# Kernel optimization log

Measured on AMD Instinct MI355X. Metric: run time of the kernel, lower is better.

The kernel has to match this reference:

```python
import jax, jax.numpy as jnp
from jax import lax
import numpy as np

EPS = 0.1          # DBSCAN radius (init arg eps)
MIN_SAMPLES = 5    # DBSCAN min_samples (init arg min_samples)
NC_MAX = 512       # fixed padded cluster budget (8 per dim * 64 dims)


def _dbscan_1d(x):
    """Exact 1-D DBSCAN on a vector x of shape (N,).
    Returns (labels, n_clusters). labels[i] in [-1, n_clusters), -1 = noise.
    Clusters are numbered in ascending value order (canonical deterministic
    relabeling of sklearn's discovery order). Border points are attached to
    the nearest core point (ties -> left)."""
    n = x.shape[0]
    order = jnp.argsort(x)
    xs = x[order]
    # core test: #points within [xs-eps, xs+eps] >= min_samples
    hi = jnp.searchsorted(xs, xs + EPS, side='right')
    lo = jnp.searchsorted(xs, xs - EPS, side='left')
    core = (hi - lo) >= MIN_SAMPLES
    inf = jnp.inf
    core_vals = jnp.where(core, xs, -inf)
    run_max = lax.cummax(core_vals, axis=0)                 # nearest core value to the left (incl self)
    prev_core_val = jnp.concatenate([jnp.full((1,), -inf, xs.dtype), run_max[:-1]])
    # a core point starts a new cluster iff no core point within eps on its left
    new_cluster = core & ((xs - prev_core_val) > EPS)
    starts = jnp.cumsum(new_cluster.astype(jnp.int32))
    cid = starts - 1                                        # cluster id carried along sorted order
    ncl = starts[-1]
    # nearest core on the left / right (values and their cluster ids)
    left_cid = lax.cummax(jnp.where(core, cid, -1), axis=0)
    left_val = run_max
    right_cid = lax.cummin(jnp.where(core, cid, n + 1), axis=0, reverse=True)
    right_val = lax.cummin(jnp.where(core, xs, inf), axis=0, reverse=True)
    dl = xs - left_val
    dr = right_val - xs
    border_cid = jnp.where(dl <= dr, left_cid, right_cid)
    border_ok = jnp.minimum(dl, dr) <= EPS
    lab_sorted = jnp.where(core, cid, jnp.where(border_ok, border_cid, -1))
    labels = jnp.zeros_like(lab_sorted).at[order].set(lab_sorted)  # unsort to original node order
    return labels, ncl


def setup_inputs() -> dict:
    key = jax.random.key(0)
    features = jax.random.normal(key, (8, 16384, 64), dtype=jnp.float32)
    return {"features": features}


def reference(features):
    B, N, D = features.shape
    xt = jnp.transpose(features, (0, 2, 1))                  # (B, D, N)
    labels, ncl = jax.vmap(jax.vmap(_dbscan_1d))(xt)         # (B, D, N), (B, D)
    off = jnp.cumsum(ncl, axis=1) - ncl                      # exclusive prefix: global cluster offset per dim
    glb = jnp.where(labels >= 0, labels + off[:, :, None], -1)
    # noise / overflow -> dump into padding column NC_MAX, sliced off below
    lbl = jnp.where(glb >= 0, jnp.minimum(glb, NC_MAX), NC_MAX)
    inc = jnp.zeros((B, N, NC_MAX + 1), features.dtype)
    b_ix = jnp.arange(B)[:, None, None]
    n_ix = jnp.arange(N)[None, None, :]
    inc = inc.at[b_ix, n_ix, lbl].set(1.0)                   # scatter cluster membership
    return inc[:, :, :NC_MAX]                                # (B, N, NC_MAX) padded incidence matrix
```

## Files before the change

kernel.cpp:

```cpp
#include <hip/hip_runtime.h>

#define NPTS   16384
#define NDIM   64
#define NBATCH 8
#define TB     1024
#define VPT    16
#define NB     8192
#define BPT    8
#define EPSF   0.1f
#define MINS   5
#define NCMAX  512
#define BIGI   0x3fffffff

__device__ __forceinline__ int phys(int i)  { return i ^ ((i >> 5) & 15); }
__device__ __forceinline__ int lphys(int i) { return i ^ (((i >> 6) & 31) << 1); }

__device__ __forceinline__ int binof(float x, float mn, float inv) {
  float fb = (x - mn) * inv;
  int b = (int)fb;
  if (fb < 0.f) b = 0;
  if (b > NB - 1) b = NB - 1;
  return b;
}

__global__ void ktrans(const float* __restrict__ f, float* __restrict__ xt) {
  __shared__ float tile[64][65];
  int blk = blockIdx.x;
  int b   = blk >> 8;
  int n0  = (blk & 255) << 6;
  for (int i = threadIdx.x; i < 64 * 64; i += 256) {
    int n = i >> 6, d = i & 63;
    tile[n][d] = f[((size_t)b * NPTS + n0 + n) * NDIM + d];
  }
  __syncthreads();
  for (int i = threadIdx.x; i < 64 * 64; i += 256) {
    int d = i >> 6, n = i & 63;
    xt[((size_t)b * NDIM + d) * NPTS + n0 + n] = tile[n][d];
  }
}

struct FS { int h; float f; float l; int li; int c; };
__device__ __forceinline__ FS fsid() { FS r; r.h = 0; r.f = 0.f; r.l = 0.f; r.li = -1; r.c = 0; return r; }
__device__ __forceinline__ FS fscomb(FS a, FS b) {
  FS r;
  r.h  = a.h | b.h;
  r.f  = a.h ? a.f : b.f;
  r.l  = b.h ? b.l : a.l;
  r.li = b.h ? b.li : a.li;
  int gap = (a.h && b.h && ((b.f - a.l) > EPSF)) ? 1 : 0;
  r.c  = a.c + b.c + gap;
  return r;
}

__global__ void __launch_bounds__(TB) kdbscan(const float* __restrict__ xt,
                                              short* __restrict__ labels,
                                              int* __restrict__ nclg) {
  const int tid  = threadIdx.x;
  const int lane = tid & 63;
  const int wid  = tid >> 6;
  const int bd   = blockIdx.x;
  const float* __restrict__ x = xt + (size_t)bd * NPTS;

  __shared__ float xs[NPTS];
  __shared__ unsigned int hist[NB];
  __shared__ unsigned int offs[NB];
  __shared__ float wmn[16], wmx[16];
  __shared__ unsigned int wsum[16];
  __shared__ int   sh[16];  __shared__ float sf[16], sl[16];
  __shared__ int   sli[16]; __shared__ int   sc[16];
  __shared__ int   wri[16]; __shared__ float wrv[16];
  short* lab = (short*)hist;

  float v[VPT];
  float mn = INFINITY, mx = -INFINITY;
  #pragma unroll
  for (int s = 0; s < VPT; ++s) {
    v[s] = x[tid + s * TB];
    mn = fminf(mn, v[s]); mx = fmaxf(mx, v[s]);
  }
  for (int d = 1; d < 64; d <<= 1) {
    mn = fminf(mn, __shfl_xor(mn, d));
    mx = fmaxf(mx, __shfl_xor(mx, d));
  }
  if (lane == 0) { wmn[wid] = mn; wmx[wid] = mx; }
  __syncthreads();
  mn = wmn[0]; mx = wmx[0];
  for (int w = 1; w < 16; ++w) { mn = fminf(mn, wmn[w]); mx = fmaxf(mx, wmx[w]); }
  float range = mx - mn;
  float inv = (range > 0.f) ? ((float)NB / range) : 0.f;

  for (int i = tid; i < NB; i += TB) hist[i] = 0u;
  __syncthreads();
  #pragma unroll
  for (int s = 0; s < VPT; ++s) atomicAdd(&hist[binof(v[s], mn, inv)], 1u);
  __syncthreads();

  unsigned int loc[BPT];
  unsigned int run = 0;
  const int bbase = tid * BPT;
  #pragma unroll
  for (int j = 0; j < BPT; ++j) { loc[j] = run; run += hist[bbase + j]; }
  unsigned int incl = run;
  for (int d = 1; d < 64; d <<= 1) {
    unsigned int u = __shfl_up(incl, d);
    if (lane >= d) incl += u;
  }
  unsigned int exc = __shfl_up(incl, 1);
  if (lane == 0) exc = 0u;
  if (lane == 63) wsum[wid] = incl;
  __syncthreads();
  unsigned int wb = 0;
  for (int w = 0; w < wid; ++w) wb += wsum[w];
  unsigned int tb0 = wb + exc;
  #pragma unroll
  for (int j = 0; j < BPT; ++j) offs[bbase + j] = tb0 + loc[j];
  __syncthreads();

  int pos[VPT];
  #pragma unroll
  for (int s = 0; s < VPT; ++s) {
    int b = binof(v[s], mn, inv);
    int p = (int)atomicAdd(&offs[b], 1u);
    pos[s] = p;
    xs[phys(p)] = v[s];
  }
  __syncthreads();

  int tgt[VPT];
  #pragma unroll
  for (int s = 0; s < VPT; ++s) {
    int b  = binof(v[s], mn, inv);
    int e0 = (int)offs[b];
    int s0 = e0 - (int)hist[b];
    float vv = v[s]; int pp = pos[s];
    int r = 0;
    for (int j = s0; j < e0; ++j) {
      float xj = xs[phys(j)];
      r += (xj < vv || (xj == vv && j < pp)) ? 1 : 0;
    }
    tgt[s] = s0 + r;
  }
  __syncthreads();
  #pragma unroll
  for (int s = 0; s < VPT; ++s) xs[phys(tgt[s])] = v[s];
  __syncthreads();

  const int p0 = tid * VPT;
  float w[VPT + 8];
  #pragma unroll
  for (int k = 0; k < VPT + 8; ++k) {
    int i = p0 - 4 + k;
    w[k] = (i < 0) ? -INFINITY : ((i >= NPTS) ? INFINITY : xs[phys(i)]);
  }
  unsigned int coremask = 0u;
  #pragma unroll
  for (int s = 0; s < VPT; ++s) {
    float xi = w[s + 4];
    float lo = xi - EPSF, hi = xi + EPSF;
    bool core = false;
    #pragma unroll
    for (int t = 0; t < MINS; ++t)
      core |= (w[s + 4 - t] >= lo) && (w[s + 8 - t] <= hi);
    if (core) coremask |= (1u << s);
  }

  FS ch = fsid();
  #pragma unroll
  for (int s = 0; s < VPT; ++s) {
    if ((coremask >> s) & 1u) {
      float xv = w[s + 4];
      if (!ch.h) { ch.h = 1; ch.f = xv; }
      else if ((xv - ch.l) > EPSF) ++ch.c;
      ch.l = xv; ch.li = p0 + s;
    }
  }
  FS cur = ch;
  for (int d = 1; d < 64; d <<= 1) {
    FS u;
    u.h  = __shfl_up(cur.h, d);
    u.f  = __shfl_up(cur.f, d);
    u.l  = __shfl_up(cur.l, d);
    u.li = __shfl_up(cur.li, d);
    u.c  = __shfl_up(cur.c, d);
    FS cmb = fscomb(u, cur);
    if (lane >= d) cur = cmb;
  }
  FS exs;
  exs.h  = __shfl_up(cur.h, 1);
  exs.f  = __shfl_up(cur.f, 1);
  exs.l  = __shfl_up(cur.l, 1);
  exs.li = __shfl_up(cur.li, 1);
  exs.c  = __shfl_up(cur.c, 1);
  if (lane == 0) exs = fsid();
  if (lane == 63) { sh[wid] = cur.h; sf[wid] = cur.f; sl[wid] = cur.l; sli[wid] = cur.li; sc[wid] = cur.c; }
  __syncthreads();
  FS pre = fsid();
  for (int w2 = 0; w2 < wid; ++w2) {
    FS t; t.h = sh[w2]; t.f = sf[w2]; t.l = sl[w2]; t.li = sli[w2]; t.c = sc[w2];
    pre = fscomb(pre, t);
  }
  FS sp = fscomb(pre, exs);

  float P  = sp.h ? sp.l  : -INFINITY;
  int   Pi = sp.h ? sp.li : -1;
  int starts = sp.h ? (sp.c + 1) : 0;
  int   li[VPT];
  float lv[VPT];
  #pragma unroll
  for (int s = 0; s < VPT; ++s) {
    int i = p0 + s;
    if ((coremask >> s) & 1u) {
      float xv = w[s + 4];
      if ((xv - P) > EPSF) ++starts;
      P = xv; Pi = i;
      lab[lphys(i)] = (short)(starts - 1);
    }
    li[s] = Pi; lv[s] = P;
  }
  if (tid == TB - 1) nclg[bd] = starts;

  int fi_ = BIGI; float fv_ = 0.f;
  #pragma unroll
  for (int s = VPT - 1; s >= 0; --s)
    if ((coremask >> s) & 1u) { fi_ = p0 + s; fv_ = w[s + 4]; }
  int ri = fi_; float rv = fv_;
  for (int d = 1; d < 64; d <<= 1) {
    int ui = __shfl_down(ri, d); float uv = __shfl_down(rv, d);
    if (lane < 64 - d && ui < ri) { ri = ui; rv = uv; }
  }
  int rei = __shfl_down(ri, 1); float rev = __shfl_down(rv, 1);
  if (lane == 63) rei = BIGI;
  if (lane == 0) { wri[wid] = ri; wrv[wid] = rv; }
  __syncthreads();
  int Ri = rei; float Rv = rev;
  for (int w2 = wid + 1; w2 < 16; ++w2)
    if (wri[w2] < Ri) { Ri = wri[w2]; Rv = wrv[w2]; }
  #pragma unroll
  for (int s = VPT - 1; s >= 0; --s) {
    int i = p0 + s;
    if ((coremask >> s) & 1u) { Ri = i; Rv = w[s + 4]; }
    else {
      float xi = w[s + 4];
      float dl = xi - lv[s];
      float dr = (Ri < NPTS) ? (Rv - xi) : INFINITY;
      short lbv = -1;
      if (fminf(dl, dr) <= EPSF)
        lbv = (dl <= dr) ? lab[lphys(li[s])] : lab[lphys(Ri)];
      lab[lphys(i)] = lbv;
    }
  }
  __syncthreads();

  #pragma unroll
  for (int s = 0; s < VPT; ++s)
    labels[(size_t)bd * NPTS + tid + s * TB] = lab[lphys(tgt[s])];
}

__global__ void koffs(const int* __restrict__ ncl, int* __restrict__ colmap) {
  int lane = threadIdx.x & 63;
  int b    = threadIdx.x >> 6;
  int vcnt = ncl[b * 64 + lane];
  int incl = vcnt;
  for (int d = 1; d < 64; d <<= 1) {
    int u = __shfl_up(incl, d);
    if (lane >= d) incl += u;
  }
  int off = incl - vcnt;
  int* cm = colmap + b * NCMAX;
  for (int k = lane; k < NCMAX; k += 64) cm[k] = -1;
  __syncthreads();
  for (int k = 0; k < vcnt; ++k) {
    int col = off + k;
    if (col < NCMAX) cm[col] = lane | (k << 8);
  }
}

__global__ void __launch_bounds__(TB) kout(const short* __restrict__ labels,
                                           const int* __restrict__ colmap,
                                           float* __restrict__ out) {
  const int tid  = threadIdx.x;
  const int lane = tid & 63;
  const int wid  = tid >> 6;
  const int b    = blockIdx.x >> 5;
  const int n0   = (blockIdx.x & 31) * 512 + wid * 32;

  int cm[8];
  const int* cmb = colmap + b * NCMAX;
  #pragma unroll
  for (int k = 0; k < 8; ++k) {
    int col = (k < 4) ? (lane * 4 + k) : (256 + lane * 4 + (k - 4));
    cm[k] = cmb[col];
  }
  const short* lb_b = labels + (size_t)b * NDIM * NPTS;

  for (int r = 0; r < 32; ++r) {
    int n = n0 + r;
    float o[8];
    #pragma unroll
    for (int k = 0; k < 8; ++k) {
      int m = cm[k];
      float val = 0.f;
      if (m >= 0) {
        int d  = m & 255;
        int kk = m >> 8;
        val = (lb_b[(size_t)d * NPTS + n] == (short)kk) ? 1.0f : 0.0f;
      }
      o[k] = val;
    }
    float4* op = (float4*)(out + ((size_t)b * NPTS + n) * NCMAX);
    op[lane]      = make_float4(o[0], o[1], o[2], o[3]);
    op[64 + lane] = make_float4(o[4], o[5], o[6], o[7]);
  }
}

extern "C" void kernel_launch(void* const* d_in, const int* in_sizes, int n_in,
                              void* d_out, int out_size, void* d_ws, size_t ws_size,
                              hipStream_t stream) {
  const float* feat = (const float*)d_in[0];
  float* out = (float*)d_out;

  char* ws = (char*)d_ws;
  float* xt     = (float*)ws;
  short* labels = (short*)(ws + (size_t)NBATCH * NPTS * NDIM * 4);
  int*   ncl    = (int*)(ws + (size_t)NBATCH * NPTS * NDIM * 4
                            + (size_t)NBATCH * NPTS * NDIM * 2);
  int*   colmap = ncl + NBATCH * NDIM;

  ktrans  <<<NBATCH * (NPTS / 64), 256, 0, stream>>>(feat, xt);
  kdbscan <<<NBATCH * NDIM, TB, 0, stream>>>(xt, labels, ncl);
  koffs   <<<1, 512, 0, stream>>>(ncl, colmap);
  kout    <<<NBATCH * 32, TB, 0, stream>>>(labels, colmap, out);
}
```

Before: 166.1 us.

## Shrink DBSCAN kernel LDS and registers to fit two blocks per CU

Histogram and offsets are packed two 16-bit counts per word, and the histogram reuses the xs buffer, which cuts shared memory per block. Label scratch moves from LDS into a global workspace buffer. The core-point window becomes a 9-element sliding register window, and the left-core index/value arrays are dropped in favour of reloading from LDS and the global label buffer. Launch bounds request more waves per EU. The aim is to raise occupancy at the cost of extra global and LDS traffic and fewer bins, which means longer in-bin rank loops.

```diff
diff --git a/kernel.cpp b/kernel.cpp
--- a/kernel.cpp
+++ b/kernel.cpp
@@ -5,15 +5,15 @@
 #define NBATCH 8
 #define TB     1024
 #define VPT    16
-#define NB     8192
-#define BPT    8
+#define NB     6144
+#define BPT    6
+#define NW     (NB/2)
 #define EPSF   0.1f
 #define MINS   5
 #define NCMAX  512
 #define BIGI   0x3fffffff
 
-__device__ __forceinline__ int phys(int i)  { return i ^ ((i >> 5) & 15); }
-__device__ __forceinline__ int lphys(int i) { return i ^ (((i >> 6) & 31) << 1); }
+__device__ __forceinline__ int phys(int i) { return i ^ ((i >> 5) & 15); }
 
 __device__ __forceinline__ int binof(float x, float mn, float inv) {
   float fb = (x - mn) * inv;
@@ -21,6 +21,9 @@
   if (fb < 0.f) b = 0;
   if (b > NB - 1) b = NB - 1;
   return b;
+}
+__device__ __forceinline__ int pk_get(unsigned w, int odd) {
+  return (int)((w >> (odd << 4)) & 0xffffu);
 }
 
 __global__ void ktrans(const float* __restrict__ f, float* __restrict__ xt) {
@@ -52,24 +55,25 @@
   return r;
 }
 
-__global__ void __launch_bounds__(TB) kdbscan(const float* __restrict__ xt,
-                                              short* __restrict__ labels,
-                                              int* __restrict__ nclg) {
+__global__ void __launch_bounds__(TB, 8) kdbscan(const float* __restrict__ xt,
+                                                 short* __restrict__ labels,
+                                                 short* __restrict__ labg,
+                                                 int* __restrict__ nclg) {
   const int tid  = threadIdx.x;
   const int lane = tid & 63;
   const int wid  = tid >> 6;
   const int bd   = blockIdx.x;
   const float* __restrict__ x = xt + (size_t)bd * NPTS;
+  short* __restrict__ lab = labg + (size_t)bd * NPTS;
 
   __shared__ float xs[NPTS];
-  __shared__ unsigned int hist[NB];
-  __shared__ unsigned int offs[NB];
+  __shared__ unsigned offsp[NW];
   __shared__ float wmn[16], wmx[16];
-  __shared__ unsigned int wsum[16];
+  __shared__ unsigned wsum[16];
   __shared__ int   sh[16];  __shared__ float sf[16], sl[16];
   __shared__ int   sli[16]; __shared__ int   sc[16];
   __shared__ int   wri[16]; __shared__ float wrv[16];
-  short* lab = (short*)hist;
+  unsigned* histp = (unsigned*)xs;
 
   float v[VPT];
   float mn = INFINITY, mx = -INFINITY;
@@ -88,39 +92,52 @@
   for (int w = 1; w < 16; ++w) { mn = fminf(mn, wmn[w]); mx = fmaxf(mx, wmx[w]); }
   float range = mx - mn;
   float inv = (range > 0.f) ? ((float)NB / range) : 0.f;
-
-  for (int i = tid; i < NB; i += TB) hist[i] = 0u;
-  __syncthreads();
-  #pragma unroll
-  for (int s = 0; s < VPT; ++s) atomicAdd(&hist[binof(v[s], mn, inv)], 1u);
-  __syncthreads();
-
-  unsigned int loc[BPT];
-  unsigned int run = 0;
+  __syncthreads();
+
+  for (int i = tid; i < NW; i += TB) histp[i] = 0u;
+  __syncthreads();
+  #pragma unroll
+  for (int s = 0; s < VPT; ++s) {
+    int b = binof(v[s], mn, inv);
+    atomicAdd(&histp[b >> 1], 1u << ((b & 1) << 4));
+  }
+  __syncthreads();
+
+  unsigned loc[BPT];
+  unsigned run = 0;
   const int bbase = tid * BPT;
   #pragma unroll
-  for (int j = 0; j < BPT; ++j) { loc[j] = run; run += hist[bbase + j]; }
-  unsigned int incl = run;
-  for (int d = 1; d < 64; d <<= 1) {
-    unsigned int u = __shfl_up(incl, d);
+  for (int j = 0; j < BPT; ++j) {
+    int b = bbase + j;
+    unsigned c = (histp[b >> 1] >> ((b & 1) << 4)) & 0xffffu;
+    loc[j] = run; run += c;
+  }
+  unsigned incl = run;
+  for (int d = 1; d < 64; d <<= 1) {
+    unsigned u = __shfl_up(incl, d);
     if (lane >= d) incl += u;
   }
-  unsigned int exc = __shfl_up(incl, 1);
+  unsigned exc = __shfl_up(incl, 1);
   if (lane == 0) exc = 0u;
   if (lane == 63) wsum[wid] = incl;
   __syncthreads();
-  unsigned int wb = 0;
+  unsigned wb = 0;
   for (int w = 0; w < wid; ++w) wb += wsum[w];
-  unsigned int tb0 = wb + exc;
-  #pragma unroll
-  for (int j = 0; j < BPT; ++j) offs[bbase + j] = tb0 + loc[j];
+  unsigned tb0 = wb + exc;
+  #pragma unroll
+  for (int k = 0; k < BPT / 2; ++k) {
+    unsigned a = tb0 + loc[2 * k];
+    unsigned b2 = tb0 + loc[2 * k + 1];
+    offsp[(bbase >> 1) + k] = a | (b2 << 16);
+  }
   __syncthreads();
 
   int pos[VPT];
   #pragma unroll
   for (int s = 0; s < VPT; ++s) {
     int b = binof(v[s], mn, inv);
-    int p = (int)atomicAdd(&offs[b], 1u);
+    unsigned old = atomicAdd(&offsp[b >> 1], 1u << ((b & 1) << 4));
+    int p = pk_get(old, b & 1);
     pos[s] = p;
     xs[phys(p)] = v[s];
   }
@@ -130,8 +147,8 @@
   #pragma unroll
   for (int s = 0; s < VPT; ++s) {
     int b  = binof(v[s], mn, inv);
-    int e0 = (int)offs[b];
-    int s0 = e0 - (int)hist[b];
+    int e0 = pk_get(offsp[b >> 1], b & 1);
+    int s0 = b ? pk_get(offsp[(b - 1) >> 1], (b - 1) & 1) : 0;
     float vv = v[s]; int pp = pos[s];
     int r = 0;
     for (int j = s0; j < e0; ++j) {
@@ -146,34 +163,36 @@
   __syncthreads();
 
   const int p0 = tid * VPT;
-  float w[VPT + 8];
-  #pragma unroll
-  for (int k = 0; k < VPT + 8; ++k) {
+  float wa[9];
+  #pragma unroll
+  for (int k = 0; k < 9; ++k) {
     int i = p0 - 4 + k;
-    w[k] = (i < 0) ? -INFINITY : ((i >= NPTS) ? INFINITY : xs[phys(i)]);
-  }
-  unsigned int coremask = 0u;
-  #pragma unroll
-  for (int s = 0; s < VPT; ++s) {
-    float xi = w[s + 4];
+    wa[k] = (i < 0) ? -INFINITY : xs[phys(i)];
+  }
+  unsigned coremask = 0u;
+  FS ch = fsid();
+  int fi = BIGI; float fv = 0.f;
+  #pragma unroll
+  for (int s = 0; s < VPT; ++s) {
+    float xi = wa[4];
     float lo = xi - EPSF, hi = xi + EPSF;
     bool core = false;
     #pragma unroll
     for (int t = 0; t < MINS; ++t)
-      core |= (w[s + 4 - t] >= lo) && (w[s + 8 - t] <= hi);
-    if (core) coremask |= (1u << s);
-  }
-
-  FS ch = fsid();
-  #pragma unroll
-  for (int s = 0; s < VPT; ++s) {
-    if ((coremask >> s) & 1u) {
-      float xv = w[s + 4];
-      if (!ch.h) { ch.h = 1; ch.f = xv; }
-      else if ((xv - ch.l) > EPSF) ++ch.c;
-      ch.l = xv; ch.li = p0 + s;
-    }
-  }
+      core |= (wa[4 - t] >= lo) && (wa[8 - t] <= hi);
+    if (core) {
+      coremask |= (1u << s);
+      if (!ch.h) { ch.h = 1; ch.f = xi; }
+      else if ((xi - ch.l) > EPSF) ++ch.c;
+      ch.l = xi; ch.li = p0 + s;
+      if (fi == BIGI) { fi = p0 + s; fv = xi; }
+    }
+    #pragma unroll
+    for (int k = 0; k < 8; ++k) wa[k] = wa[k + 1];
+    int nx = p0 + s + 5;
+    wa[8] = (nx < NPTS) ? xs[phys(nx)] : INFINITY;
+  }
+
   FS cur = ch;
   for (int d = 1; d < 64; d <<= 1) {
     FS u;
@@ -204,26 +223,22 @@
   float P  = sp.h ? sp.l  : -INFINITY;
   int   Pi = sp.h ? sp.li : -1;
   int starts = sp.h ? (sp.c + 1) : 0;
-  int   li[VPT];
-  float lv[VPT];
   #pragma unroll
   for (int s = 0; s < VPT; ++s) {
     int i = p0 + s;
     if ((coremask >> s) & 1u) {
-      float xv = w[s + 4];
+      float xv = xs[phys(i)];
       if ((xv - P) > EPSF) ++starts;
       P = xv; Pi = i;
-      lab[lphys(i)] = (short)(starts - 1);
-    }
-    li[s] = Pi; lv[s] = P;
+      lab[i] = (short)(starts - 1);
+    } else {
+      lab[i] = (short)Pi;
+    }
   }
   if (tid == TB - 1) nclg[bd] = starts;
-
-  int fi_ = BIGI; float fv_ = 0.f;
-  #pragma unroll
-  for (int s = VPT - 1; s >= 0; --s)
-    if ((coremask >> s) & 1u) { fi_ = p0 + s; fv_ = w[s + 4]; }
-  int ri = fi_; float rv = fv_;
+  __syncthreads();
+
+  int ri = fi; float rv = fv;
   for (int d = 1; d < 64; d <<= 1) {
     int ui = __shfl_down(ri, d); float uv = __shfl_down(rv, d);
     if (lane < 64 - d && ui < ri) { ri = ui; rv = uv; }
@@ -235,25 +250,27 @@
   int Ri = rei; float Rv = rev;
   for (int w2 = wid + 1; w2 < 16; ++w2)
     if (wri[w2] < Ri) { Ri = wri[w2]; Rv = wrv[w2]; }
+
   #pragma unroll
   for (int s = VPT - 1; s >= 0; --s) {
     int i = p0 + s;
-    if ((coremask >> s) & 1u) { Ri = i; Rv = w[s + 4]; }
+    if ((coremask >> s) & 1u) { Ri = i; Rv = xs[phys(i)]; }
     else {
-      float xi = w[s + 4];
-      float dl = xi - lv[s];
+      float xi = xs[phys(i)];
+      int li_ = (int)lab[i];
+      float dl = (li_ >= 0) ? (xi - xs[phys(li_)]) : INFINITY;
       float dr = (Ri < NPTS) ? (Rv - xi) : INFINITY;
       short lbv = -1;
       if (fminf(dl, dr) <= EPSF)
-        lbv = (dl <= dr) ? lab[lphys(li[s])] : lab[lphys(Ri)];
-      lab[lphys(i)] = lbv;
+        lbv = (dl <= dr) ? lab[li_] : lab[Ri];
+      lab[i] = lbv;
     }
   }
   __syncthreads();
 
   #pragma unroll
   for (int s = 0; s < VPT; ++s)
-    labels[(size_t)bd * NPTS + tid + s * TB] = lab[lphys(tgt[s])];
+    labels[(size_t)bd * NPTS + tid + s * TB] = lab[tgt[s]];
 }
 
 __global__ void koffs(const int* __restrict__ ncl, int* __restrict__ colmap) {
@@ -320,14 +337,16 @@
   float* out = (float*)d_out;
 
   char* ws = (char*)d_ws;
+  size_t xt_b   = (size_t)NBATCH * NPTS * NDIM * 4;
+  size_t lbl_b  = (size_t)NBATCH * NPTS * NDIM * 2;
   float* xt     = (float*)ws;
-  short* labels = (short*)(ws + (size_t)NBATCH * NPTS * NDIM * 4);
-  int*   ncl    = (int*)(ws + (size_t)NBATCH * NPTS * NDIM * 4
-                            + (size_t)NBATCH * NPTS * NDIM * 2);
+  short* labels = (short*)(ws + xt_b);
+  short* labg   = (short*)(ws + xt_b + lbl_b);
+  int*   ncl    = (int*)(ws + xt_b + 2 * lbl_b);
   int*   colmap = ncl + NBATCH * NDIM;
 
   ktrans  <<<NBATCH * (NPTS / 64), 256, 0, stream>>>(feat, xt);
-  kdbscan <<<NBATCH * NDIM, TB, 0, stream>>>(xt, labels, ncl);
+  kdbscan <<<NBATCH * NDIM, TB, 0, stream>>>(xt, labels, labg, ncl);
   koffs   <<<1, 512, 0, stream>>>(ncl, colmap);
   kout    <<<NBATCH * 32, TB, 0, stream>>>(labels, colmap, out);
 }
```

After: 241.2 us. 45.3% more time.
